# Optimization experiments

Measured on AMD Instinct MI355X. Metric: run time of the kernel, lower is better.

## Reference

```python
import jax, jax.numpy as jnp
import numpy as np

N_NODES = 50000
N_EDGES = 800000
F_IN = 64
F_OUT = 64
EPS = 1e-5


def setup_inputs() -> dict:
    key = jax.random.key(0)
    ks = jax.random.split(key, 6)
    x = jax.random.normal(ks[0], (N_NODES, F_IN), dtype=jnp.float32)
    edge_index = jax.random.randint(ks[1], (2, N_EDGES), 0, N_NODES, dtype=jnp.int64)
    # pre MLP: Linear(2*F_in -> F_in); post MLP: Linear(13*F_in -> F_out); lin: Linear(F_out -> F_out)
    pre_w = jax.random.normal(ks[2], (2 * F_IN, F_IN), dtype=jnp.float32) / np.sqrt(2 * F_IN)
    pre_b = jnp.zeros((F_IN,), dtype=jnp.float32)
    post_w = jax.random.normal(ks[3], (13 * F_IN, F_OUT), dtype=jnp.float32) / np.sqrt(13 * F_IN)
    post_b = jnp.zeros((F_OUT,), dtype=jnp.float32)
    lin_w = jax.random.normal(ks[4], (F_OUT, F_OUT), dtype=jnp.float32) / np.sqrt(F_OUT)
    lin_b = jnp.zeros((F_OUT,), dtype=jnp.float32)
    return {"x": x, "edge_index": edge_index, "pre_w": pre_w, "pre_b": pre_b,
            "post_w": post_w, "post_b": post_b, "lin_w": lin_w, "lin_b": lin_b}


def _pna_conv(x, edge_index, pre_w, pre_b, post_w, post_b, lin_w, lin_b):
    n = x.shape[0]
    src = edge_index[0]  # x_j (source / neighbor)
    dst = edge_index[1]  # x_i (target / aggregation index)

    # message: pre-MLP on [x_i, x_j]  -> [E, F_in]
    h = jnp.concatenate([x[dst], x[src]], axis=-1)  # [E, 2*F_in]
    m = h @ pre_w + pre_b                            # [E, F_in]

    # degree of each target node
    deg = jax.ops.segment_sum(jnp.ones_like(src, dtype=x.dtype), dst, num_segments=n)  # [N]
    has_nb = deg > 0
    deg_c = jnp.maximum(deg, 1.0)[:, None]  # clamp(1), [N,1]

    # aggregators: mean, min, max, std (single pass over edges per reduction)
    s1 = jax.ops.segment_sum(m, dst, num_segments=n)
    s2 = jax.ops.segment_sum(m * m, dst, num_segments=n)
    mean = s1 / deg_c
    mean_sq = s2 / deg_c
    std = jnp.sqrt(jax.nn.relu(mean_sq - mean * mean) + EPS)
    mn = jax.ops.segment_min(m, dst, num_segments=n)
    mx = jax.ops.segment_max(m, dst, num_segments=n)
    mn = jnp.where(has_nb[:, None], mn, 0.0)
    mx = jnp.where(has_nb[:, None], mx, 0.0)
    aggs = jnp.concatenate([mean, mn, mx, std], axis=-1)  # [N, 4*F_in]

    # degree scalers: identity, amplification, attenuation
    # avg log-degree from the graph's degree histogram (log(deg+1), unclamped)
    avg_deg_log = jnp.mean(jnp.log(deg + 1.0))
    deg_log = jnp.log(deg_c + 1.0)  # uses clamped degree, [N,1]
    amp = deg_log / avg_deg_log
    att = avg_deg_log / deg_log
    scaled = jnp.concatenate([aggs, aggs * amp, aggs * att], axis=-1)  # [N, 12*F_in]

    # post MLP on [x, aggregated] then final linear
    out = jnp.concatenate([x, scaled], axis=-1)  # [N, 13*F_in]
    out = out @ post_w + post_b                  # [N, F_out]
    out = out @ lin_w + lin_b                    # [N, F_out]
    return out


def reference(x, edge_index, pre_w, pre_b, post_w, post_b, lin_w, lin_b):
    # eval-mode forward: dropout is identity, no loss branch
    return _pna_conv(x, edge_index, pre_w, pre_b, post_w, post_b, lin_w, lin_b)
```

## Files before the change

### kernel.cpp

```cpp
#include <hip/hip_runtime.h>
#include <math.h>
#include <stdint.h>

#define EPS 1e-5f

typedef __attribute__((ext_vector_type(8))) short bf16x8;
typedef __attribute__((ext_vector_type(4))) float f32x4;

union FragU {
    bf16x8 v;
    ushort u[8];
};

__device__ __forceinline__ ushort f2bf(float f)
{
    union { float f; uint u; } v; v.f = f;
    uint r = v.u + 0x7FFF + ((v.u >> 16) & 1);
    return (ushort)(r >> 16);
}
__device__ __forceinline__ float bf2f(ushort u)
{
    union { uint u; float f; } v; v.u = (uint)u << 16;
    return v.f;
}
__device__ __forceinline__ uint packbf2(float lo, float hi)
{
    return (uint)f2bf(lo) | ((uint)f2bf(hi) << 16);
}

#define MFMA(a, b, c) __builtin_amdgcn_mfma_f32_16x16x32_bf16((a), (b), (c), 0, 0, 0)

#define PART_BLOCKS 128

__global__ __launch_bounds__(64) void k_fuse_pack(
    const float* __restrict__ post_w, const float* __restrict__ post_b,
    const float* __restrict__ lin_w, const float* __restrict__ lin_b,
    ushort* __restrict__ Wp, float* __restrict__ bc)
{
    int r = blockIdx.x, j = threadIdx.x;
    if (r < 832) {
        float acc = 0.f;
        for (int k = 0; k < 64; ++k)
            acc = fmaf(post_w[r * 64 + k], lin_w[k * 64 + j], acc);
        int tile, kk;
        if (r < 64) { tile = (r >> 5) * 4 + (j >> 4); kk = r & 31; }
        else {
            int g = (r - 64) >> 8, ka = (r - 64) & 255;
            tile = 8 + (g * 8 + (ka >> 5)) * 4 + (j >> 4); kk = ka & 31;
        }
        int lane = (j & 15) | ((kk >> 3) << 4);
        Wp[tile * 512 + lane * 8 + (kk & 7)] = f2bf(acc);
    } else {
        float a = lin_b[j];
        for (int k = 0; k < 64; ++k)
            a = fmaf(post_b[k], lin_w[k * 64 + j], a);
        bc[j] = a;
    }
}

__global__ __launch_bounds__(256) void k_preh(
    const float* __restrict__ x, const float* __restrict__ pre_w,
    const float* __restrict__ pre_b, const int* __restrict__ ei,
    float* __restrict__ Af, ushort* __restrict__ Bb,
    int* __restrict__ hist, int N, int E, int NWB)
{
    int t = threadIdx.x;
    if (blockIdx.x >= NWB) {
        __shared__ int lh[256];
        int blk = blockIdx.x - NWB;
        lh[t] = 0;
        __syncthreads();
        int chunk = (E + PART_BLOCKS - 1) / PART_BLOCKS;
        int c0 = blk * chunk, c1 = min(E, c0 + chunk);
        for (int e = c0 + t; e < c1; e += 256) {
            int dst = ei[E + e];
            if ((unsigned)dst < (unsigned)N) atomicAdd(&lh[dst >> 8], 1);
        }
        __syncthreads();
        hist[blk * 256 + t] = lh[t];
        return;
    }

    __shared__ ushort pw[16 * 512];
    for (int idx = t; idx < 8192; idx += 256) {
        int kin = idx >> 7, o = idx & 127;
        float v = (o < 64) ? pre_w[kin * 64 + o]
                           : pre_w[(64 + kin) * 64 + (o - 64)];
        int kk = kin & 31;
        int tile = (kin >> 5) * 8 + (o >> 4);
        int ln = (o & 15) | ((kk >> 3) << 4);
        pw[tile * 512 + ln * 8 + (kk & 7)] = f2bf(v);
    }
    __syncthreads();

    int w = t >> 6, lane = t & 63;
    int nb = (blockIdx.x * 4 + w) * 32;
    if (nb >= N) return;
    int lr = lane & 15, lk = lane >> 4;

    f32x4 acc[2][8] = {};
#pragma unroll
    for (int ks = 0; ks < 2; ++ks) {
        FragU A0, A1;
        {
            int r0 = min(nb + lr, N - 1);
            int r1 = min(nb + 16 + lr, N - 1);
            const float* p0 = &x[r0 * 64 + ks * 32 + lk * 8];
            const float* p1 = &x[r1 * 64 + ks * 32 + lk * 8];
            float4 a0 = *reinterpret_cast<const float4*>(p0);
            float4 a1 = *reinterpret_cast<const float4*>(p0 + 4);
            float4 c0 = *reinterpret_cast<const float4*>(p1);
            float4 c1 = *reinterpret_cast<const float4*>(p1 + 4);
            A0.u[0] = f2bf(a0.x); A0.u[1] = f2bf(a0.y);
            A0.u[2] = f2bf(a0.z); A0.u[3] = f2bf(a0.w);
            A0.u[4] = f2bf(a1.x); A0.u[5] = f2bf(a1.y);
            A0.u[6] = f2bf(a1.z); A0.u[7] = f2bf(a1.w);
            A1.u[0] = f2bf(c0.x); A1.u[1] = f2bf(c0.y);
            A1.u[2] = f2bf(c0.z); A1.u[3] = f2bf(c0.w);
            A1.u[4] = f2bf(c1.x); A1.u[5] = f2bf(c1.y);
            A1.u[6] = f2bf(c1.z); A1.u[7] = f2bf(c1.w);
        }
#pragma unroll
        for (int jt = 0; jt < 8; ++jt) {
            bf16x8 B = *reinterpret_cast<const bf16x8*>(
                &pw[(ks * 8 + jt) * 512 + lane * 8]);
            acc[0][jt] = MFMA(A0.v, B, acc[0][jt]);
            acc[1][jt] = MFMA(A1.v, B, acc[1][jt]);
        }
    }
#pragma unroll
    for (int mt = 0; mt < 2; ++mt)
#pragma unroll
        for (int jt = 0; jt < 8; ++jt) {
            int o = jt * 16 + lr;
#pragma unroll
            for (int rg = 0; rg < 4; ++rg) {
                int r = nb + mt * 16 + lk * 4 + rg;
                if (r < N) {
                    float v = acc[mt][jt][rg];
                    if (o < 64) Af[r * 64 + o] = v + pre_b[o];
                    else        Bb[r * 64 + (o - 64)] = f2bf(v);
                }
            }
        }
}

__global__ __launch_bounds__(256) void k_cscan(
    const int* __restrict__ hist, int* __restrict__ colscan,
    int* __restrict__ bucketStart, int* __restrict__ offsets,
    float* __restrict__ avg_acc, int N)
{
    __shared__ int ws[4];
    int b = threadIdx.x;
    if (b == 0) *avg_acc = 0.f;

    int run = 0;
    for (int base = 0; base < PART_BLOCKS; base += 8) {
        int h[8];
#pragma unroll
        for (int k = 0; k < 8; ++k) h[k] = hist[(base + k) * 256 + b];
#pragma unroll
        for (int k = 0; k < 8; ++k) {
            colscan[(base + k) * 256 + b] = run;
            run += h[k];
        }
    }

    int lane = b & 63, wv = b >> 6;
    int inc = run;
#pragma unroll
    for (int off = 1; off < 64; off <<= 1) {
        int u = __shfl_up(inc, off);
        if (lane >= off) inc += u;
    }
    if (lane == 63) ws[wv] = inc;
    __syncthreads();
    int add = 0;
#pragma unroll
    for (int i = 0; i < 4; ++i)
        if (i < wv) add += ws[i];
    int incl = inc + add;
    bucketStart[b] = incl - run;
    if (b == 255) {
        bucketStart[256] = incl;
        offsets[N] = incl;
    }
}

__global__ __launch_bounds__(256) void k_part(
    const int* __restrict__ ei, const int* __restrict__ colscan,
    const int* __restrict__ bucketStart, uint* __restrict__ staged,
    int E, int N)
{
    __shared__ int cur[256];
    int t = threadIdx.x, blk = blockIdx.x;
    cur[t] = bucketStart[t] + colscan[blk * 256 + t];
    __syncthreads();
    int chunk = (E + PART_BLOCKS - 1) / PART_BLOCKS;
    int c0 = blk * chunk, c1 = min(E, c0 + chunk);
    for (int e = c0 + t; e < c1; e += 256) {
        int src = ei[e];
        int dst = ei[E + e];
        if ((unsigned)dst < (unsigned)N) {
            if ((unsigned)src >= (unsigned)N) src = 0;
            int pos = atomicAdd(&cur[dst >> 8], 1);
            staged[pos] = (uint)src | ((uint)(dst & 255) << 16);
        }
    }
}

__global__ __launch_bounds__(256) void k_place(
    const uint* __restrict__ staged, const int* __restrict__ bucketStart,
    int* __restrict__ csr_src, int* __restrict__ offsets,
    float* __restrict__ avg_acc, int N)
{
    __shared__ int cnt[256];
    __shared__ int wsum[4];
    __shared__ float fl[4];
    int t = threadIdx.x, lane = t & 63, wv = t >> 6;
    int b = blockIdx.x;
    int s0 = bucketStart[b], s1 = bucketStart[b + 1];

    cnt[t] = 0;
    __syncthreads();
    for (int i = s0 + t; i < s1; i += 256)
        atomicAdd(&cnt[(staged[i] >> 16) & 255], 1);
    __syncthreads();

    int d = cnt[t];
    int v = d;
#pragma unroll
    for (int off = 1; off < 64; off <<= 1) {
        int u = __shfl_up(v, off);
        if (lane >= off) v += u;
    }
    if (lane == 63) wsum[wv] = v;
    __syncthreads();
    int wvoff = 0;
#pragma unroll
    for (int i = 0; i < 4; ++i)
        if (i < wv) wvoff += wsum[i];
    int excl = wvoff + v - d;

    int node = b * 256 + t;
    if (node < N) offsets[node] = s0 + excl;

    float sl = (node < N) ? logf((float)d + 1.0f) : 0.f;
    for (int off = 32; off; off >>= 1) sl += __shfl_down(sl, off);
    if (lane == 0) fl[wv] = sl;

    cnt[t] = excl;
    __syncthreads();
    if (t == 0) atomicAdd(avg_acc, fl[0] + fl[1] + fl[2] + fl[3]);

    for (int i = s0 + t; i < s1; i += 256) {
        uint ev = staged[i];
        int p = atomicAdd(&cnt[(ev >> 16) & 255], 1);
        csr_src[s0 + p] = (int)(ev & 0xFFFFu);
    }
}

__global__ __launch_bounds__(256) void k_aggregate(
    const float* __restrict__ Af, const ushort* __restrict__ Bb,
    const int* __restrict__ offsets, const int* __restrict__ csr_src,
    const float* __restrict__ avg_sum, ushort* __restrict__ aggs,
    float* __restrict__ amp, float* __restrict__ att, int N)
{
    int wave = threadIdx.x >> 6, lane = threadIdx.x & 63;
    int n = blockIdx.x * 4 + wave;
    if (n >= N) return;

    int off0 = offsets[n], off1 = offsets[n + 1];
    int d = off1 - off0;
    int hl = lane & 31;
    int which = lane >> 5;

    float2 a2 = *reinterpret_cast<const float2*>(&Af[(size_t)n * 64 + hl * 2]);

    float s0 = 0.f, s1 = 0.f, q0 = 0.f, q1 = 0.f;
    float mn0 = 3.4e38f, mn1 = 3.4e38f, mx0 = -3.4e38f, mx1 = -3.4e38f;

#define UPD(bv)                                                         \
    {                                                                   \
        float m0 = a2.x + bf2f((ushort)((bv) & 0xFFFFu));               \
        float m1 = a2.y + bf2f((ushort)((bv) >> 16));                   \
        s0 += m0; q0 = fmaf(m0, m0, q0);                                \
        mn0 = fminf(mn0, m0); mx0 = fmaxf(mx0, m0);                     \
        s1 += m1; q1 = fmaf(m1, m1, q1);                                \
        mn1 = fminf(mn1, m1); mx1 = fmaxf(mx1, m1);                     \
    }

    for (int base = off0; base < off1; base += 64) {
        int cnt = min(64, off1 - base);
        int s_idx = 0;
        if (lane < cnt) s_idx = csr_src[base + lane];
        int i = 0;
        for (; i + 7 < cnt; i += 8) {
            int sA = __shfl(s_idx, i + 0 + which);
            int sB = __shfl(s_idx, i + 2 + which);
            int sC = __shfl(s_idx, i + 4 + which);
            int sD = __shfl(s_idx, i + 6 + which);
            uint bA = *reinterpret_cast<const uint*>(&Bb[(size_t)sA * 64 + hl * 2]);
            uint bB = *reinterpret_cast<const uint*>(&Bb[(size_t)sB * 64 + hl * 2]);
            uint bC = *reinterpret_cast<const uint*>(&Bb[(size_t)sC * 64 + hl * 2]);
            uint bD = *reinterpret_cast<const uint*>(&Bb[(size_t)sD * 64 + hl * 2]);
            UPD(bA); UPD(bB); UPD(bC); UPD(bD);
        }
        for (; i < cnt; i += 2) {
            int sj = __shfl(s_idx, i + which);
            uint bv = *reinterpret_cast<const uint*>(&Bb[(size_t)sj * 64 + hl * 2]);
            if ((which == 0) | (i + 1 < cnt)) UPD(bv);
        }
    }
#undef UPD

    s0 += __shfl_xor(s0, 32);  s1 += __shfl_xor(s1, 32);
    q0 += __shfl_xor(q0, 32);  q1 += __shfl_xor(q1, 32);
    mn0 = fminf(mn0, __shfl_xor(mn0, 32));
    mn1 = fminf(mn1, __shfl_xor(mn1, 32));
    mx0 = fmaxf(mx0, __shfl_xor(mx0, 32));
    mx1 = fmaxf(mx1, __shfl_xor(mx1, 32));

    float dc = (d > 0) ? (float)d : 1.0f;
    float mean0 = s0 / dc, mean1 = s1 / dc;
    float std0 = sqrtf(fmaxf(q0 / dc - mean0 * mean0, 0.f) + EPS);
    float std1 = sqrtf(fmaxf(q1 / dc - mean1 * mean1, 0.f) + EPS);
    if (d == 0) { mn0 = 0.f; mn1 = 0.f; mx0 = 0.f; mx1 = 0.f; }

    if (lane < 32) {
        uint* ag = reinterpret_cast<uint*>(&aggs[(size_t)n * 256]);
        ag[0 * 32 + hl] = packbf2(mean0, mean1);
        ag[1 * 32 + hl] = packbf2(mn0, mn1);
        ag[2 * 32 + hl] = packbf2(mx0, mx1);
        ag[3 * 32 + hl] = packbf2(std0, std1);
    }
    if (lane == 0) {
        float avg = *avg_sum / (float)N;
        float dlog = logf(dc + 1.0f);
        amp[n] = dlog / avg;
        att[n] = avg / dlog;
    }
}

__global__ __launch_bounds__(256) void k_out_gemm(
    const float* __restrict__ x, const ushort* __restrict__ aggs,
    const float* __restrict__ amp, const float* __restrict__ att,
    const ushort* __restrict__ Wp, const float* __restrict__ bc,
    float* __restrict__ out, int N)
{
    int w = threadIdx.x >> 6, lane = threadIdx.x & 63;
    int nb = (blockIdx.x * 4 + w) * 32;
    int lr = lane & 15, lk = lane >> 4;

    f32x4 accP[2][4] = {};
    f32x4 accA[2][4] = {};
    f32x4 accT[2][4] = {};

#pragma unroll
    for (int ks = 0; ks < 2; ++ks) {
        FragU A0, A1;
        {
            int r0 = min(nb + lr, N - 1);
            int r1 = min(nb + 16 + lr, N - 1);
            const float* p0 = &x[r0 * 64 + ks * 32 + lk * 8];
            const float* p1 = &x[r1 * 64 + ks * 32 + lk * 8];
            float4 a0 = *reinterpret_cast<const float4*>(p0);
            float4 a1 = *reinterpret_cast<const float4*>(p0 + 4);
            float4 c0 = *reinterpret_cast<const float4*>(p1);
            float4 c1 = *reinterpret_cast<const float4*>(p1 + 4);
            A0.u[0] = f2bf(a0.x); A0.u[1] = f2bf(a0.y);
            A0.u[2] = f2bf(a0.z); A0.u[3] = f2bf(a0.w);
            A0.u[4] = f2bf(a1.x); A0.u[5] = f2bf(a1.y);
            A0.u[6] = f2bf(a1.z); A0.u[7] = f2bf(a1.w);
            A1.u[0] = f2bf(c0.x); A1.u[1] = f2bf(c0.y);
            A1.u[2] = f2bf(c0.z); A1.u[3] = f2bf(c0.w);
            A1.u[4] = f2bf(c1.x); A1.u[5] = f2bf(c1.y);
            A1.u[6] = f2bf(c1.z); A1.u[7] = f2bf(c1.w);
        }
#pragma unroll
        for (int jt = 0; jt < 4; ++jt) {
            bf16x8 B = *reinterpret_cast<const bf16x8*>(
                &Wp[(ks * 4 + jt) * 512 + lane * 8]);
            accP[0][jt] = MFMA(A0.v, B, accP[0][jt]);
            accP[1][jt] = MFMA(A1.v, B, accP[1][jt]);
        }
    }

#pragma unroll 2
    for (int ks = 0; ks < 8; ++ks) {
        bf16x8 A0 = *reinterpret_cast<const bf16x8*>(
            &aggs[(size_t)(nb + lr) * 256 + ks * 32 + lk * 8]);
        bf16x8 A1 = *reinterpret_cast<const bf16x8*>(
            &aggs[(size_t)(nb + 16 + lr) * 256 + ks * 32 + lk * 8]);
        bf16x8 B0[4], B1[4], B2[4];
#pragma unroll
        for (int jt = 0; jt < 4; ++jt) {
            B0[jt] = *reinterpret_cast<const bf16x8*>(
                &Wp[(8 + (0 * 8 + ks) * 4 + jt) * 512 + lane * 8]);
            B1[jt] = *reinterpret_cast<const bf16x8*>(
                &Wp[(8 + (1 * 8 + ks) * 4 + jt) * 512 + lane * 8]);
            B2[jt] = *reinterpret_cast<const bf16x8*>(
                &Wp[(8 + (2 * 8 + ks) * 4 + jt) * 512 + lane * 8]);
        }
#pragma unroll
        for (int jt = 0; jt < 4; ++jt) {
            accP[0][jt] = MFMA(A0, B0[jt], accP[0][jt]);
            accP[1][jt] = MFMA(A1, B0[jt], accP[1][jt]);
            accA[0][jt] = MFMA(A0, B1[jt], accA[0][jt]);
            accA[1][jt] = MFMA(A1, B1[jt], accA[1][jt]);
            accT[0][jt] = MFMA(A0, B2[jt], accT[0][jt]);
            accT[1][jt] = MFMA(A1, B2[jt], accT[1][jt]);
        }
    }

#pragma unroll
    for (int mt = 0; mt < 2; ++mt) {
        int rb = nb + mt * 16 + lk * 4;
        float am[4], at[4];
#pragma unroll
        for (int rg = 0; rg < 4; ++rg) {
            am[rg] = amp[rb + rg];
            at[rg] = att[rb + rg];
        }
#pragma unroll
        for (int jt = 0; jt < 4; ++jt) {
            int j = jt * 16 + lr;
            float b = bc[j];
#pragma unroll
            for (int rg = 0; rg < 4; ++rg) {
                int r = rb + rg;
                if (r < N) {
                    out[(size_t)r * 64 + j] =
                        accP[mt][jt][rg] + am[rg] * accA[mt][jt][rg] +
                        at[rg] * accT[mt][jt][rg] + b;
                }
            }
        }
    }
}

static inline char* alignup(char* p, size_t a)
{
    return (char*)(((uintptr_t)p + a - 1) & ~(uintptr_t)(a - 1));
}

extern "C" void kernel_launch(void* const* d_in, const int* in_sizes, int n_in,
                              void* d_out, int out_size, void* d_ws, size_t ws_size,
                              hipStream_t stream)
{
    const float* x      = (const float*)d_in[0];
    const int*   ei     = (const int*)d_in[1];
    const float* pre_w  = (const float*)d_in[2];
    const float* pre_b  = (const float*)d_in[3];
    const float* post_w = (const float*)d_in[4];
    const float* post_b = (const float*)d_in[5];
    const float* lin_w  = (const float*)d_in[6];
    const float* lin_b  = (const float*)d_in[7];
    float* out = (float*)d_out;

    const int N = in_sizes[0] / 64;
    const int E = in_sizes[1] / 2;
    const int Npad = (N + 127) & ~127;
    const int NWB = Npad / 128;
    const int NBUCK = (N + 255) >> 8;
    if (N > 65536) return;

    size_t need = 0;
    auto acct = [&](size_t bytes) { need = ((need + 255) & ~(size_t)255) + bytes; };
    acct((size_t)N * 64 * 4);
    acct((size_t)N * 64 * 2);
    acct((size_t)Npad * 256 * 2);
    acct(104 * 512 * 2);
    acct(64 * 4);
    acct((size_t)Npad * 4);
    acct((size_t)Npad * 4);
    acct(((size_t)N + 1) * 4);
    acct((size_t)E * 4);
    acct((size_t)E * 4);
    acct(PART_BLOCKS * 256 * 4);
    acct(PART_BLOCKS * 256 * 4);
    acct(257 * 4);
    acct(4);
    if (ws_size < need) return;

    char* p = (char*)d_ws;
    auto take = [&](size_t bytes) {
        p = alignup(p, 256);
        void* r = (void*)p;
        p += bytes;
        return r;
    };
    float*  Af        = (float*)take((size_t)N * 64 * 4);
    ushort* Bb        = (ushort*)take((size_t)N * 64 * 2);
    ushort* aggs      = (ushort*)take((size_t)Npad * 256 * 2);
    ushort* Wp        = (ushort*)take(104 * 512 * 2);
    float*  bc        = (float*)take(64 * 4);
    float*  amp       = (float*)take((size_t)Npad * 4);
    float*  att       = (float*)take((size_t)Npad * 4);
    int*    offsets   = (int*)take(((size_t)N + 1) * 4);
    int*    csr_src   = (int*)take((size_t)E * 4);
    uint*   staged    = (uint*)take((size_t)E * 4);
    int*    hist      = (int*)take(PART_BLOCKS * 256 * 4);
    int*    colscan   = (int*)take(PART_BLOCKS * 256 * 4);
    int*    bstart    = (int*)take(257 * 4);
    float*  avg_acc   = (float*)take(4);

    k_preh<<<NWB + PART_BLOCKS, 256, 0, stream>>>(x, pre_w, pre_b, ei,
                                                  Af, Bb, hist, N, E, NWB);
    k_fuse_pack<<<833, 64, 0, stream>>>(post_w, post_b, lin_w, lin_b, Wp, bc);
    k_cscan<<<1, 256, 0, stream>>>(hist, colscan, bstart, offsets, avg_acc, N);
    k_part<<<PART_BLOCKS, 256, 0, stream>>>(ei, colscan, bstart, staged, E, N);
    k_place<<<NBUCK, 256, 0, stream>>>(staged, bstart, csr_src, offsets,
                                       avg_acc, N);
    k_aggregate<<<(N + 3) / 4, 256, 0, stream>>>(Af, Bb, offsets, csr_src,
                                                 avg_acc, aggs, amp, att, N);
    k_out_gemm<<<NWB, 256, 0, stream>>>(x, aggs, amp, att, Wp, bc, out, N);
}
```

Measured before the change: 186.0 us.

## Fuse weight packing into pre kernel, shrink CSR and A to 16-bit, hoist A

```diff
diff --git a/kernel.cpp b/kernel.cpp
--- a/kernel.cpp
+++ b/kernel.cpp
@@ -31,40 +31,45 @@
 #define MFMA(a, b, c) __builtin_amdgcn_mfma_f32_16x16x32_bf16((a), (b), (c), 0, 0, 0)
 
 #define PART_BLOCKS 128
-
-__global__ __launch_bounds__(64) void k_fuse_pack(
-    const float* __restrict__ post_w, const float* __restrict__ post_b,
-    const float* __restrict__ lin_w, const float* __restrict__ lin_b,
-    ushort* __restrict__ Wp, float* __restrict__ bc)
-{
-    int r = blockIdx.x, j = threadIdx.x;
-    if (r < 832) {
-        float acc = 0.f;
-        for (int k = 0; k < 64; ++k)
-            acc = fmaf(post_w[r * 64 + k], lin_w[k * 64 + j], acc);
-        int tile, kk;
-        if (r < 64) { tile = (r >> 5) * 4 + (j >> 4); kk = r & 31; }
-        else {
-            int g = (r - 64) >> 8, ka = (r - 64) & 255;
-            tile = 8 + (g * 8 + (ka >> 5)) * 4 + (j >> 4); kk = ka & 31;
-        }
-        int lane = (j & 15) | ((kk >> 3) << 4);
-        Wp[tile * 512 + lane * 8 + (kk & 7)] = f2bf(acc);
-    } else {
-        float a = lin_b[j];
-        for (int k = 0; k < 64; ++k)
-            a = fmaf(post_b[k], lin_w[k * 64 + j], a);
-        bc[j] = a;
-    }
-}
+#define FP_BLOCKS   209
 
 __global__ __launch_bounds__(256) void k_preh(
     const float* __restrict__ x, const float* __restrict__ pre_w,
     const float* __restrict__ pre_b, const int* __restrict__ ei,
-    float* __restrict__ Af, ushort* __restrict__ Bb,
-    int* __restrict__ hist, int N, int E, int NWB)
+    const float* __restrict__ post_w, const float* __restrict__ post_b,
+    const float* __restrict__ lin_w, const float* __restrict__ lin_b,
+    ushort* __restrict__ Ab, ushort* __restrict__ Bb,
+    int* __restrict__ hist, ushort* __restrict__ Wp, float* __restrict__ bc,
+    int N, int E, int NWB)
 {
     int t = threadIdx.x;
+
+    if (blockIdx.x >= NWB + PART_BLOCKS) {
+        int unit = (blockIdx.x - NWB - PART_BLOCKS) * 4 + (t >> 6);
+        int j = t & 63;
+        if (unit > 832) return;
+        if (unit < 832) {
+            int r = unit;
+            float acc = 0.f;
+            for (int k = 0; k < 64; ++k)
+                acc = fmaf(post_w[r * 64 + k], lin_w[k * 64 + j], acc);
+            int tile, kk;
+            if (r < 64) { tile = (r >> 5) * 4 + (j >> 4); kk = r & 31; }
+            else {
+                int g = (r - 64) >> 8, ka = (r - 64) & 255;
+                tile = 8 + (g * 8 + (ka >> 5)) * 4 + (j >> 4); kk = ka & 31;
+            }
+            int ln = (j & 15) | ((kk >> 3) << 4);
+            Wp[tile * 512 + ln * 8 + (kk & 7)] = f2bf(acc);
+        } else {
+            float a = lin_b[j];
+            for (int k = 0; k < 64; ++k)
+                a = fmaf(post_b[k], lin_w[k * 64 + j], a);
+            bc[j] = a;
+        }
+        return;
+    }
+
     if (blockIdx.x >= NWB) {
         __shared__ int lh[256];
         int blk = blockIdx.x - NWB;
@@ -138,7 +143,7 @@
                 int r = nb + mt * 16 + lk * 4 + rg;
                 if (r < N) {
                     float v = acc[mt][jt][rg];
-                    if (o < 64) Af[r * 64 + o] = v + pre_b[o];
+                    if (o < 64) Ab[r * 64 + o] = f2bf(v + pre_b[o]);
                     else        Bb[r * 64 + (o - 64)] = f2bf(v);
                 }
             }
@@ -211,7 +216,7 @@
 
 __global__ __launch_bounds__(256) void k_place(
     const uint* __restrict__ staged, const int* __restrict__ bucketStart,
-    int* __restrict__ csr_src, int* __restrict__ offsets,
+    ushort* __restrict__ csr16, int* __restrict__ offsets,
     float* __restrict__ avg_acc, int N)
 {
     __shared__ int cnt[256];
@@ -256,13 +261,13 @@
     for (int i = s0 + t; i < s1; i += 256) {
         uint ev = staged[i];
         int p = atomicAdd(&cnt[(ev >> 16) & 255], 1);
-        csr_src[s0 + p] = (int)(ev & 0xFFFFu);
+        csr16[s0 + p] = (ushort)(ev & 0xFFFFu);
     }
 }
 
 __global__ __launch_bounds__(256) void k_aggregate(
-    const float* __restrict__ Af, const ushort* __restrict__ Bb,
-    const int* __restrict__ offsets, const int* __restrict__ csr_src,
+    const ushort* __restrict__ Ab, const ushort* __restrict__ Bb,
+    const int* __restrict__ offsets, const ushort* __restrict__ csr16,
     const float* __restrict__ avg_sum, ushort* __restrict__ aggs,
     float* __restrict__ amp, float* __restrict__ att, int N)
 {
@@ -275,15 +280,13 @@
     int hl = lane & 31;
     int which = lane >> 5;
 
-    float2 a2 = *reinterpret_cast<const float2*>(&Af[(size_t)n * 64 + hl * 2]);
-
     float s0 = 0.f, s1 = 0.f, q0 = 0.f, q1 = 0.f;
     float mn0 = 3.4e38f, mn1 = 3.4e38f, mx0 = -3.4e38f, mx1 = -3.4e38f;
 
 #define UPD(bv)                                                         \
     {                                                                   \
-        float m0 = a2.x + bf2f((ushort)((bv) & 0xFFFFu));               \
-        float m1 = a2.y + bf2f((ushort)((bv) >> 16));                   \
+        float m0 = bf2f((ushort)((bv) & 0xFFFFu));                      \
+        float m1 = bf2f((ushort)((bv) >> 16));                          \
         s0 += m0; q0 = fmaf(m0, m0, q0);                                \
         mn0 = fminf(mn0, m0); mx0 = fmaxf(mx0, m0);                     \
         s1 += m1; q1 = fmaf(m1, m1, q1);                                \
@@ -293,8 +296,28 @@
     for (int base = off0; base < off1; base += 64) {
         int cnt = min(64, off1 - base);
         int s_idx = 0;
-        if (lane < cnt) s_idx = csr_src[base + lane];
+        if (lane < cnt) s_idx = (int)csr16[base + lane];
         int i = 0;
+        for (; i + 15 < cnt; i += 16) {
+            int sA = __shfl(s_idx, i + 0 + which);
+            int sB = __shfl(s_idx, i + 2 + which);
+            int sC = __shfl(s_idx, i + 4 + which);
+            int sD = __shfl(s_idx, i + 6 + which);
+            int sE = __shfl(s_idx, i + 8 + which);
+            int sF = __shfl(s_idx, i + 10 + which);
+            int sG = __shfl(s_idx, i + 12 + which);
+            int sH = __shfl(s_idx, i + 14 + which);
+            uint bA = *reinterpret_cast<const uint*>(&Bb[(size_t)sA * 64 + hl * 2]);
+            uint bB = *reinterpret_cast<const uint*>(&Bb[(size_t)sB * 64 + hl * 2]);
+            uint bC = *reinterpret_cast<const uint*>(&Bb[(size_t)sC * 64 + hl * 2]);
+            uint bD = *reinterpret_cast<const uint*>(&Bb[(size_t)sD * 64 + hl * 2]);
+            uint bE = *reinterpret_cast<const uint*>(&Bb[(size_t)sE * 64 + hl * 2]);
+            uint bF = *reinterpret_cast<const uint*>(&Bb[(size_t)sF * 64 + hl * 2]);
+            uint bG = *reinterpret_cast<const uint*>(&Bb[(size_t)sG * 64 + hl * 2]);
+            uint bH = *reinterpret_cast<const uint*>(&Bb[(size_t)sH * 64 + hl * 2]);
+            UPD(bA); UPD(bB); UPD(bC); UPD(bD);
+            UPD(bE); UPD(bF); UPD(bG); UPD(bH);
+        }
         for (; i + 7 < cnt; i += 8) {
             int sA = __shfl(s_idx, i + 0 + which);
             int sB = __shfl(s_idx, i + 2 + which);
@@ -321,17 +344,28 @@
     mx0 = fmaxf(mx0, __shfl_xor(mx0, 32));
     mx1 = fmaxf(mx1, __shfl_xor(mx1, 32));
 
+    uint av = *reinterpret_cast<const uint*>(&Ab[(size_t)n * 64 + hl * 2]);
+    float a0 = bf2f((ushort)(av & 0xFFFFu));
+    float a1 = bf2f((ushort)(av >> 16));
+
     float dc = (d > 0) ? (float)d : 1.0f;
-    float mean0 = s0 / dc, mean1 = s1 / dc;
-    float std0 = sqrtf(fmaxf(q0 / dc - mean0 * mean0, 0.f) + EPS);
-    float std1 = sqrtf(fmaxf(q1 / dc - mean1 * mean1, 0.f) + EPS);
-    if (d == 0) { mn0 = 0.f; mn1 = 0.f; mx0 = 0.f; mx1 = 0.f; }
+    float mB0 = s0 / dc, mB1 = s1 / dc;
+    float std0 = sqrtf(fmaxf(q0 / dc - mB0 * mB0, 0.f) + EPS);
+    float std1 = sqrtf(fmaxf(q1 / dc - mB1 * mB1, 0.f) + EPS);
+    float mean0 = a0 + mB0, mean1 = a1 + mB1;
+    float mnF0 = a0 + mn0, mnF1 = a1 + mn1;
+    float mxF0 = a0 + mx0, mxF1 = a1 + mx1;
+    if (d == 0) {
+        mean0 = mean1 = 0.f;
+        mnF0 = mnF1 = 0.f;
+        mxF0 = mxF1 = 0.f;
+    }
 
     if (lane < 32) {
         uint* ag = reinterpret_cast<uint*>(&aggs[(size_t)n * 256]);
         ag[0 * 32 + hl] = packbf2(mean0, mean1);
-        ag[1 * 32 + hl] = packbf2(mn0, mn1);
-        ag[2 * 32 + hl] = packbf2(mx0, mx1);
+        ag[1 * 32 + hl] = packbf2(mnF0, mnF1);
+        ag[2 * 32 + hl] = packbf2(mxF0, mxF1);
         ag[3 * 32 + hl] = packbf2(std0, std1);
     }
     if (lane == 0) {
@@ -467,7 +501,7 @@
 
     size_t need = 0;
     auto acct = [&](size_t bytes) { need = ((need + 255) & ~(size_t)255) + bytes; };
-    acct((size_t)N * 64 * 4);
+    acct((size_t)N * 64 * 2);
     acct((size_t)N * 64 * 2);
     acct((size_t)Npad * 256 * 2);
     acct(104 * 512 * 2);
@@ -475,7 +509,7 @@
     acct((size_t)Npad * 4);
     acct((size_t)Npad * 4);
     acct(((size_t)N + 1) * 4);
-    acct((size_t)E * 4);
+    acct((size_t)E * 2);
     acct((size_t)E * 4);
     acct(PART_BLOCKS * 256 * 4);
     acct(PART_BLOCKS * 256 * 4);
@@ -490,7 +524,7 @@
         p += bytes;
         return r;
     };
-    float*  Af        = (float*)take((size_t)N * 64 * 4);
+    ushort* Ab        = (ushort*)take((size_t)N * 64 * 2);
     ushort* Bb        = (ushort*)take((size_t)N * 64 * 2);
     ushort* aggs      = (ushort*)take((size_t)Npad * 256 * 2);
     ushort* Wp        = (ushort*)take(104 * 512 * 2);
@@ -498,21 +532,21 @@
     float*  amp       = (float*)take((size_t)Npad * 4);
     float*  att       = (float*)take((size_t)Npad * 4);
     int*    offsets   = (int*)take(((size_t)N + 1) * 4);
-    int*    csr_src   = (int*)take((size_t)E * 4);
+    ushort* csr16     = (ushort*)take((size_t)E * 2);
     uint*   staged    = (uint*)take((size_t)E * 4);
     int*    hist      = (int*)take(PART_BLOCKS * 256 * 4);
     int*    colscan   = (int*)take(PART_BLOCKS * 256 * 4);
     int*    bstart    = (int*)take(257 * 4);
     float*  avg_acc   = (float*)take(4);
 
-    k_preh<<<NWB + PART_BLOCKS, 256, 0, stream>>>(x, pre_w, pre_b, ei,
-                                                  Af, Bb, hist, N, E, NWB);
-    k_fuse_pack<<<833, 64, 0, stream>>>(post_w, post_b, lin_w, lin_b, Wp, bc);
+    k_preh<<<NWB + PART_BLOCKS + FP_BLOCKS, 256, 0, stream>>>(
+        x, pre_w, pre_b, ei, post_w, post_b, lin_w, lin_b,
+        Ab, Bb, hist, Wp, bc, N, E, NWB);
     k_cscan<<<1, 256, 0, stream>>>(hist, colscan, bstart, offsets, avg_acc, N);
     k_part<<<PART_BLOCKS, 256, 0, stream>>>(ei, colscan, bstart, staged, E, N);
-    k_place<<<NBUCK, 256, 0, stream>>>(staged, bstart, csr_src, offsets,
+    k_place<<<NBUCK, 256, 0, stream>>>(staged, bstart, csr16, offsets,
                                        avg_acc, N);
-    k_aggregate<<<(N + 3) / 4, 256, 0, stream>>>(Af, Bb, offsets, csr_src,
+    k_aggregate<<<(N + 3) / 4, 256, 0, stream>>>(Ab, Bb, offsets, csr16,
                                                  avg_acc, aggs, amp, att, N);
     k_out_gemm<<<NWB, 256, 0, stream>>>(x, aggs, amp, att, Wp, bc, out, N);
 }
```

New measurement: 181.9 us. 2.2% less time.
